# Kernel optimization log

Hardware: AMD Instinct MI355X
Metric: run time of the kernel (lower is better)

The kernel has to match this reference:

```python
import jax, jax.numpy as jnp
import numpy as np

# fixed ontology layer output sizes (edge_index[-1].max()+1 in the original)
NUM_OUT = (5000, 1000, 256)


def setup_inputs() -> dict:
    key = jax.random.key(0)
    ks = jax.random.split(key, 12)
    B, F0 = 1024, 20000
    sizes_in = (20000, 5000, 1000)
    n_edges = (100000, 50000, 10000)
    inp = {
        "data": jax.random.normal(ks[0], (B, F0), dtype=jnp.float32),
        "p0": jax.random.normal(ks[1], (sizes_in[0],), dtype=jnp.float32),
        "p1": jax.random.normal(ks[2], (sizes_in[1],), dtype=jnp.float32),
        "p2": jax.random.normal(ks[3], (sizes_in[2],), dtype=jnp.float32),
        "W": jax.random.normal(ks[4], (10, NUM_OUT[-1]), dtype=jnp.float32) * (2.0 / (10 + NUM_OUT[-1])) ** 0.5,
        "b": jnp.zeros((10,), dtype=jnp.float32),
    }
    rng = np.random.default_rng(0)
    for i, (nin, nout, ne) in enumerate(zip(sizes_in, NUM_OUT, n_edges)):
        src = rng.integers(0, nin, size=ne).astype(np.int32)
        dst = rng.integers(0, nout, size=ne).astype(np.int32)
        dst[:nout] = np.arange(nout, dtype=np.int32)  # ensure every output node gets >=1 edge
        inp[f"src{i}"] = jnp.asarray(src)
        inp[f"dst{i}"] = jnp.asarray(dst)
    return inp


def _layer(x, p, src, dst, num_out):
    # elementwise scale -> gather along feature dim -> scatter-mean -> relu
    t = x * p  # [B, Fin]
    lifted = t[:, src]  # [B, E]
    sums = jnp.zeros((x.shape[0], num_out), x.dtype).at[:, dst].add(lifted)
    cnt = jnp.zeros((num_out,), x.dtype).at[dst].add(1.0)
    return jax.nn.relu(sums / jnp.maximum(cnt, 1.0))


def reference(data, p0, p1, p2, W, b, src0, dst0, src1, dst1, src2, dst2):
    x = _layer(data, p0, src0, dst0, NUM_OUT[0])
    x = _layer(x, p1, src1, dst1, NUM_OUT[1])
    x = _layer(x, p2, src2, dst2, NUM_OUT[2])
    out = x @ W.T + b  # Linear(256, 10)
    return jnp.squeeze(out, -1) if out.shape[-1] == 1 else out
```

## Files before the change

kernel.cpp:

```cpp
#include <hip/hip_runtime.h>
#include <hip/hip_fp16.h>

constexpr int Bsz   = 1024;
constexpr int F0    = 20000;
constexpr int NOUT0 = 5000, NOUT1 = 1000, NOUT2 = 256;
constexpr int NE0   = 100000, NE1 = 50000, NE2 = 10000;
constexpr int CNT_N  = NOUT0 + NOUT1 + NOUT2;
constexpr int OFFS_N = CNT_N + 3;
constexpr int CSR_N  = NE0 + NE1 + NE2;
constexpr int MAXIDX = 512;
constexpr int NTILE_F = (F0 + 63) / 64;
constexpr int NTILE   = NTILE_F * (Bsz / 64);
constexpr int SCB     = (CSR_N + 255) / 256;
constexpr int NSLICE  = 8;
constexpr int SLW     = Bsz / NSLICE;

union H4 { uint2 u; __half2 h[2]; };

__global__ __launch_bounds__(256) void count_edges(
    const int* __restrict__ dst0, const int* __restrict__ dst1,
    const int* __restrict__ dst2, int* __restrict__ cnt)
{
    const int i = blockIdx.x * 256 + threadIdx.x;
    if (i < NE0)                 atomicAdd(&cnt[dst0[i]], 1);
    else if (i < NE0 + NE1)      atomicAdd(&cnt[NOUT0 + dst1[i - NE0]], 1);
    else if (i < CSR_N)          atomicAdd(&cnt[NOUT0 + NOUT1 + dst2[i - NE0 - NE1]], 1);
}

__global__ __launch_bounds__(1024) void scan_offs(
    const int* __restrict__ cnt, int* __restrict__ offs, int* __restrict__ cursor)
{
    const int L = blockIdx.x;
    const int t = threadIdx.x;
    const int n  = (L == 0) ? NOUT0 : (L == 1) ? NOUT1 : NOUT2;
    const int cb = (L == 0) ? 0 : (L == 1) ? NOUT0 : NOUT0 + NOUT1;
    const int ob = (L == 0) ? 0 : (L == 1) ? NOUT0 + 1 : NOUT0 + NOUT1 + 2;
    const int* c = cnt + cb;
    int* ofs = offs + ob;
    int* cur = cursor + cb;

    __shared__ int sc[1024];
    constexpr int CH = 5;
    const int base = t * CH;
    int vals[CH];
    int local = 0;
#pragma unroll
    for (int k = 0; k < CH; ++k) {
        const int i = base + k;
        const int v = (i < n) ? c[i] : 0;
        vals[k] = v; local += v;
    }
    sc[t] = local;
    __syncthreads();
    for (int d = 1; d < 1024; d <<= 1) {
        const int v = (t >= d) ? sc[t - d] : 0;
        __syncthreads();
        sc[t] += v;
        __syncthreads();
    }
    int excl = sc[t] - local;
#pragma unroll
    for (int k = 0; k < CH; ++k) {
        const int i = base + k;
        if (i < n) { ofs[i] = excl; cur[i] = excl; }
        excl += vals[k];
    }
    if (t == 1023) ofs[n] = sc[1023];
}

__global__ __launch_bounds__(256) void transpose_scatter(
    const float* __restrict__ data, const float* __restrict__ p0,
    __half* __restrict__ dataT,
    const int* __restrict__ src0, const int* __restrict__ dst0,
    const int* __restrict__ src1, const int* __restrict__ dst1,
    const int* __restrict__ src2, const int* __restrict__ dst2,
    int* __restrict__ cursor, int* __restrict__ csr)
{
    const int t = threadIdx.x;
    const int bid = blockIdx.x;
    if (bid < NTILE) {
        __shared__ float tile[64][65];
        const int c0 = (bid % NTILE_F) * 64;
        const int r0 = (bid / NTILE_F) * 64;
        const int f4 = t & 15, rr = t >> 4;
        const int col = c0 + f4 * 4;
        if (col < F0) {
#pragma unroll
            for (int p = 0; p < 4; ++p) {
                const int br = rr + p * 16;
                const float4 v = *(const float4*)&data[(size_t)(r0 + br) * F0 + col];
                tile[br][f4 * 4 + 0] = v.x; tile[br][f4 * 4 + 1] = v.y;
                tile[br][f4 * 4 + 2] = v.z; tile[br][f4 * 4 + 3] = v.w;
            }
        }
        __syncthreads();
        const int b4 = t & 15, fr = t >> 4;
#pragma unroll
        for (int p = 0; p < 4; ++p) {
            const int f = c0 + fr + p * 16;
            if (f < F0) {
                const float s = p0[f];
                H4 o;
                o.h[0] = __floats2half2_rn(tile[b4 * 4 + 0][fr + p * 16] * s,
                                           tile[b4 * 4 + 1][fr + p * 16] * s);
                o.h[1] = __floats2half2_rn(tile[b4 * 4 + 2][fr + p * 16] * s,
                                           tile[b4 * 4 + 3][fr + p * 16] * s);
                *(uint2*)&dataT[(size_t)f * Bsz + r0 + b4 * 4] = o.u;
            }
        }
    } else {
        const int i = (bid - NTILE) * 256 + t;
        if (i < NE0) {
            const int pos = atomicAdd(&cursor[dst0[i]], 1);
            csr[pos] = src0[i];
        } else if (i < NE0 + NE1) {
            const int k = i - NE0;
            const int pos = atomicAdd(&cursor[NOUT0 + dst1[k]], 1);
            csr[NE0 + pos] = src1[k];
        } else if (i < CSR_N) {
            const int k = i - NE0 - NE1;
            const int pos = atomicAdd(&cursor[NOUT0 + NOUT1 + dst2[k]], 1);
            csr[NE0 + NE1 + pos] = src2[k];
        }
    }
}

template<int LAYER>
__global__ __launch_bounds__(64) void layer_slice(
    const __half* __restrict__ xT, const int* __restrict__ csr,
    const int* __restrict__ offs, const float* __restrict__ pnext,
    __half* __restrict__ yT)
{
    __shared__ int sidx[MAXIDX];
    const int bid = blockIdx.x;
    const int slice = bid & (NSLICE - 1);
    const int j = bid >> 3;
    const int t = threadIdx.x;
    const int beg = offs[j], end = offs[j + 1];
    const int n = end - beg;
    const int np = n < MAXIDX ? n : MAXIDX;
    for (int i = t; i < np; i += 64) sidx[i] = csr[beg + i];
    __syncthreads();

    const int c = slice * SLW + t * 2;
    float a0x = 0.f, a0y = 0.f, a1x = 0.f, a1y = 0.f;
    float a2x = 0.f, a2y = 0.f, a3x = 0.f, a3y = 0.f;
    int e = 0;
    for (; e + 4 <= np; e += 4) {
        const __half2 v0 = *(const __half2*)&xT[(size_t)sidx[e + 0] * Bsz + c];
        const __half2 v1 = *(const __half2*)&xT[(size_t)sidx[e + 1] * Bsz + c];
        const __half2 v2 = *(const __half2*)&xT[(size_t)sidx[e + 2] * Bsz + c];
        const __half2 v3 = *(const __half2*)&xT[(size_t)sidx[e + 3] * Bsz + c];
        const float2 f0 = __half22float2(v0);
        const float2 f1 = __half22float2(v1);
        const float2 f2 = __half22float2(v2);
        const float2 f3 = __half22float2(v3);
        a0x += f0.x; a0y += f0.y; a1x += f1.x; a1y += f1.y;
        a2x += f2.x; a2y += f2.y; a3x += f3.x; a3y += f3.y;
    }
    for (; e < np; ++e) {
        const float2 f = __half22float2(*(const __half2*)&xT[(size_t)sidx[e] * Bsz + c]);
        a0x += f.x; a0y += f.y;
    }
    for (int ee = MAXIDX; ee < n; ++ee) {
        const float2 f = __half22float2(*(const __half2*)&xT[(size_t)csr[beg + ee] * Bsz + c]);
        a0x += f.x; a0y += f.y;
    }
    const float ax = a0x + a1x + a2x + a3x;
    const float ay = a0y + a1y + a2y + a3y;

    const float inv = 1.0f / fmaxf((float)n, 1.0f);
    const float sc = (pnext ? pnext[j] : 1.0f) * inv;
    const __half2 o = __floats2half2_rn(fmaxf(ax, 0.f) * sc, fmaxf(ay, 0.f) * sc);
    *(__half2*)&yT[(size_t)j * Bsz + c] = o;
}

__global__ __launch_bounds__(256) void head_gemm(
    const __half* __restrict__ y2T, const float* __restrict__ W,
    const float* __restrict__ bias, float* __restrict__ out)
{
    __shared__ float ws[10 * 256];
    __shared__ float bs[10];
    const int t = threadIdx.x;
    for (int i = t; i < 10 * 256; i += 256) ws[i] = W[i];
    if (t < 10) bs[t] = bias[t];
    __syncthreads();

    const int b = blockIdx.x * 256 + t;
    float acc[10];
#pragma unroll
    for (int o = 0; o < 10; ++o) acc[o] = bs[o];
    for (int k = 0; k < 256; ++k) {
        const float v = __half2float(y2T[(size_t)k * Bsz + b]);
#pragma unroll
        for (int o = 0; o < 10; ++o) acc[o] += v * ws[o * 256 + k];
    }
#pragma unroll
    for (int o = 0; o < 10; ++o) out[(size_t)b * 10 + o] = acc[o];
}

extern "C" void kernel_launch(void* const* d_in, const int* in_sizes, int n_in,
                              void* d_out, int out_size, void* d_ws, size_t ws_size,
                              hipStream_t stream)
{
    const float* data = (const float*)d_in[0];
    const float* p0   = (const float*)d_in[1];
    const float* p1   = (const float*)d_in[2];
    const float* p2   = (const float*)d_in[3];
    const float* W    = (const float*)d_in[4];
    const float* bias = (const float*)d_in[5];
    const int* src0 = (const int*)d_in[6];
    const int* dst0 = (const int*)d_in[7];
    const int* src1 = (const int*)d_in[8];
    const int* dst1 = (const int*)d_in[9];
    const int* src2 = (const int*)d_in[10];
    const int* dst2 = (const int*)d_in[11];

    char* ws = (char*)d_ws;
    auto align = [](size_t x) { return (x + 255) & ~size_t(255); };
    size_t o = 0;
    __half* dataT = (__half*)(ws + o); o = align(o + (size_t)F0 * Bsz * 2);
    __half* y0    = (__half*)(ws + o); o = align(o + (size_t)NOUT0 * Bsz * 2);
    __half* y1    = (__half*)(ws + o); o = align(o + (size_t)NOUT1 * Bsz * 2);
    __half* y2    = (__half*)(ws + o); o = align(o + (size_t)NOUT2 * Bsz * 2);
    int* cnt      = (int*)(ws + o);    o = align(o + (size_t)CNT_N * 4);
    int* offs     = (int*)(ws + o);    o = align(o + (size_t)OFFS_N * 4);
    int* cursor   = (int*)(ws + o);    o = align(o + (size_t)CNT_N * 4);
    int* csr      = (int*)(ws + o);    o = align(o + (size_t)CSR_N * 4);

    hipMemsetAsync(cnt, 0, (size_t)CNT_N * 4, stream);
    count_edges<<<SCB, 256, 0, stream>>>(dst0, dst1, dst2, cnt);
    scan_offs<<<3, 1024, 0, stream>>>(cnt, offs, cursor);
    transpose_scatter<<<NTILE + SCB, 256, 0, stream>>>(
        data, p0, dataT, src0, dst0, src1, dst1, src2, dst2, cursor, csr);
    layer_slice<0><<<NOUT0 * NSLICE, 64, 0, stream>>>(dataT, csr, offs, p1, y0);
    layer_slice<1><<<NOUT1 * NSLICE, 64, 0, stream>>>(y0, csr + NE0, offs + NOUT0 + 1, p2, y1);
    layer_slice<2><<<NOUT2 * NSLICE, 64, 0, stream>>>(y1, csr + NE0 + NE1,
                                                      offs + NOUT0 + NOUT1 + 2, nullptr, y2);
    head_gemm<<<Bsz / 256, 256, 0, stream>>>(y2, W, bias, (float*)d_out);
}
```

Before: 117.7 us.

## Split layer-0 gather into two batch-half launches with edge-parallel half-waves

```diff
diff --git a/kernel.cpp b/kernel.cpp
--- a/kernel.cpp
+++ b/kernel.cpp
@@ -125,6 +125,65 @@
     }
 }
 
+template<int HALF>
+__global__ __launch_bounds__(64) void layer0_slice(
+    const __half* __restrict__ xT, const int* __restrict__ csr,
+    const int* __restrict__ offs, const float* __restrict__ p1,
+    __half* __restrict__ y0)
+{
+    __shared__ int sidx[MAXIDX];
+    const int bid = blockIdx.x;
+    const int slice = bid & (NSLICE - 1);
+    const int j = bid >> 3;
+    const int t = threadIdx.x;
+    const int beg = offs[j], end = offs[j + 1];
+    const int n = end - beg;
+    const int np = n < MAXIDX ? n : MAXIDX;
+    for (int i = t; i < np; i += 64) sidx[i] = csr[beg + i];
+    __syncthreads();
+
+    const int c  = HALF * 512 + slice * 64 + (t & 31) * 2;
+    const int ep = t >> 5;
+    float a0x = 0.f, a0y = 0.f, a1x = 0.f, a1y = 0.f;
+    float a2x = 0.f, a2y = 0.f, a3x = 0.f, a3y = 0.f;
+    int e = 0;
+    for (; e + 8 <= np; e += 8) {
+        const int s0 = sidx[e + 0 + ep];
+        const int s1 = sidx[e + 2 + ep];
+        const int s2 = sidx[e + 4 + ep];
+        const int s3 = sidx[e + 6 + ep];
+        const float2 f0 = __half22float2(*(const __half2*)&xT[(size_t)s0 * Bsz + c]);
+        const float2 f1 = __half22float2(*(const __half2*)&xT[(size_t)s1 * Bsz + c]);
+        const float2 f2 = __half22float2(*(const __half2*)&xT[(size_t)s2 * Bsz + c]);
+        const float2 f3 = __half22float2(*(const __half2*)&xT[(size_t)s3 * Bsz + c]);
+        a0x += f0.x; a0y += f0.y; a1x += f1.x; a1y += f1.y;
+        a2x += f2.x; a2y += f2.y; a3x += f3.x; a3y += f3.y;
+    }
+    for (; e < np; e += 2) {
+        const int idx = e + ep;
+        const float m = (idx < np) ? 1.f : 0.f;
+        const int s = sidx[(idx < np) ? idx : 0];
+        const float2 f = __half22float2(*(const __half2*)&xT[(size_t)s * Bsz + c]);
+        a0x += m * f.x; a0y += m * f.y;
+    }
+    for (int ee = MAXIDX; ee < n; ++ee) {
+        const float m = (ep == 0) ? 1.f : 0.f;
+        const float2 f = __half22float2(*(const __half2*)&xT[(size_t)csr[beg + ee] * Bsz + c]);
+        a0x += m * f.x; a0y += m * f.y;
+    }
+    float ax = a0x + a1x + a2x + a3x;
+    float ay = a0y + a1y + a2y + a3y;
+    ax += __shfl_xor(ax, 32);
+    ay += __shfl_xor(ay, 32);
+
+    if (t < 32) {
+        const float inv = 1.0f / fmaxf((float)n, 1.0f);
+        const float sc = p1[j] * inv;
+        *(__half2*)&y0[(size_t)j * Bsz + c] =
+            __floats2half2_rn(fmaxf(ax, 0.f) * sc, fmaxf(ay, 0.f) * sc);
+    }
+}
+
 template<int LAYER>
 __global__ __launch_bounds__(64) void layer_slice(
     const __half* __restrict__ xT, const int* __restrict__ csr,
@@ -233,7 +292,8 @@
     scan_offs<<<3, 1024, 0, stream>>>(cnt, offs, cursor);
     transpose_scatter<<<NTILE + SCB, 256, 0, stream>>>(
         data, p0, dataT, src0, dst0, src1, dst1, src2, dst2, cursor, csr);
-    layer_slice<0><<<NOUT0 * NSLICE, 64, 0, stream>>>(dataT, csr, offs, p1, y0);
+    layer0_slice<0><<<NOUT0 * NSLICE, 64, 0, stream>>>(dataT, csr, offs, p1, y0);
+    layer0_slice<1><<<NOUT0 * NSLICE, 64, 0, stream>>>(dataT, csr, offs, p1, y0);
     layer_slice<1><<<NOUT1 * NSLICE, 64, 0, stream>>>(y0, csr + NE0, offs + NOUT0 + 1, p2, y1);
     layer_slice<2><<<NOUT2 * NSLICE, 64, 0, stream>>>(y1, csr + NE0 + NE1,
                                                       offs + NOUT0 + NOUT1 + 2, nullptr, y2);
```

After: 127.2 us. 8.1% more time.
